# Kernel optimization log

Measured on AMD Instinct MI355X. Metric: run time of the kernel, lower is better.

Reference implementation:

```python
import jax, jax.numpy as jnp
import numpy as np

N_NODES = 50000
N_EDGES = 600000
CHANNELS = 128
HEADS = 8


def setup_inputs() -> dict:
    key = jax.random.key(0)
    k1, k2, k3 = jax.random.split(key, 3)
    x = jax.random.normal(k1, (N_NODES, CHANNELS), dtype=jnp.float32)
    edge_index = jax.random.randint(k2, (2, N_EDGES), 0, N_NODES, dtype=jnp.int32)
    att = jax.random.normal(k3, (HEADS, 2 * (CHANNELS // HEADS)), dtype=jnp.float32)
    return {"x": x, "edge_index": edge_index, "att": att}


def reference(x, edge_index, att):
    # x: [N, C], edge_index: [2, E], att: [H, 2*D] with D = C // H
    src, dst = edge_index[0], edge_index[1]
    n = x.shape[0]
    h = att.shape[0]
    d = att.shape[1] // 2

    x_src = x[src].reshape(-1, h, d)   # [E, H, D]
    x_dst = x[dst].reshape(-1, h, d)   # [E, H, D]

    # (cat([x_src, x_dst]) * att).sum(-1) == x_src @ att[:, :D] + x_dst @ att[:, D:]
    a_src, a_dst = att[:, :d], att[:, d:]
    alpha = jnp.einsum('ehd,hd->eh', x_src, a_src) + jnp.einsum('ehd,hd->eh', x_dst, a_dst)
    alpha = jnp.where(alpha >= 0, alpha, 0.2 * alpha)  # LeakyReLU(0.2)

    # segment softmax over dst; torch scatter_reduce amax includes the zero init,
    # so the per-node max is max(segment_max, 0)
    seg_max = jax.ops.segment_max(alpha, dst, num_segments=n)  # [N, H]
    seg_max = jnp.maximum(seg_max, 0.0)
    alpha = jnp.exp(alpha - seg_max[dst])
    seg_sum = jax.ops.segment_sum(alpha, dst, num_segments=n)  # [N, H]
    alpha = alpha / jnp.maximum(seg_sum[dst], 1e-10)

    # weighted scatter-add of source features
    weighted = x_src * alpha[..., None]                        # [E, H, D]
    out = jax.ops.segment_sum(weighted, dst, num_segments=n)   # [N, H, D]
    return out.reshape(n, -1)
```

## Files before the change

kernel.cpp:

```cpp
#include <hip/hip_runtime.h>

#define N_NODES  50000
#define N_EDGES  600000
#define CHANNELS 128
#define HEADS    8
#define HEAD_DIM 16
#define CAP      64
#define CSTRIDE  4

#define PREP_BLOCK 256
#define SCAT_GRID  ((N_EDGES + PREP_BLOCK - 1) / PREP_BLOCK)
#define LOGIT_GRID ((N_NODES * CHANNELS) / PREP_BLOCK)
#define WPB        4

__global__ void prep_kernel(const float* __restrict__ x,
                            const float* __restrict__ att,
                            const int*   __restrict__ src,
                            const int*   __restrict__ dst,
                            int*            __restrict__ cursor,
                            unsigned short* __restrict__ bucket,
                            float*          __restrict__ ls8,
                            float*          __restrict__ ld8,
                            unsigned short* __restrict__ xb) {
    int b = blockIdx.x;
    if (b < SCAT_GRID) {
        int e = b * PREP_BLOCK + threadIdx.x;
        if (e < N_EDGES) {
            int d = dst[e];
            int pos = atomicAdd(&cursor[d * CSTRIDE], 1);
            if (pos < CAP) bucket[(size_t)d * CAP + pos] = (unsigned short)src[e];
        }
    } else {
        int gid = (b - SCAT_GRID) * PREP_BLOCK + threadIdx.x;
        int n = gid >> 7;
        int c = gid & 127;
        int h = c >> 4;
        int j = c & 15;
        float v = x[gid];

        unsigned int u = __float_as_uint(v);
        xb[gid] = (unsigned short)((u + 0x7FFFu + ((u >> 16) & 1u)) >> 16);

        float ts = v * att[h * (2 * HEAD_DIM) + j];
        float td = v * att[h * (2 * HEAD_DIM) + HEAD_DIM + j];
#pragma unroll
        for (int o = 8; o >= 1; o >>= 1) {
            ts += __shfl_xor(ts, o, 16);
            td += __shfl_xor(td, o, 16);
        }
        if (j == 0) {
            ls8[n * HEADS + h] = ts;
            ld8[n * HEADS + h] = td;
        }
    }
}

__global__ void fused_gat_kernel(const unsigned short* __restrict__ xb,
                                 const float* __restrict__ ls8,
                                 const float* __restrict__ ld8,
                                 const int*   __restrict__ cursor,
                                 const unsigned short* __restrict__ bucket,
                                 float*       __restrict__ out) {
    __shared__ float s_a[WPB * CAP * HEADS];

    int wave = threadIdx.x >> 6;
    int lane = threadIdx.x & 63;
    int n = blockIdx.x * WPB + wave;
    if (n >= N_NODES) return;
    int h = lane >> 3;
    int j = lane & 7;

    int   cnt_raw = cursor[n * CSTRIDE];
    int   myidx   = (int)bucket[(size_t)n * CAP + lane];
    float ldst    = ld8[n * HEADS + h];
    int cnt = (cnt_raw > CAP) ? CAP : cnt_raw;

    float* sa = s_a + wave * (CAP * HEADS);

    float mymax = -1e30f;
    for (int i = j; i < cnt; i += 8) {
        int   s  = __shfl(myidx, i);
        float lg = ls8[s * HEADS + h] + ldst;
        float a  = (lg >= 0.0f) ? lg : 0.2f * lg;
        sa[i * HEADS + h] = a;
        mymax = fmaxf(mymax, a);
    }
#pragma unroll
    for (int o = 4; o >= 1; o >>= 1) mymax = fmaxf(mymax, __shfl_xor(mymax, o, 8));
    float m = fmaxf(mymax, 0.0f);

    float l = 0.0f, accx = 0.0f, accy = 0.0f;
    unsigned int q0 = 0, q1 = 0, q2 = 0;
    if (cnt > 0) {
        int s0 = __shfl(myidx, 0);
        q0 = ((const unsigned int*)(xb + (size_t)s0 * CHANNELS))[lane];
    }
    if (cnt > 1) {
        int s1 = __shfl(myidx, 1);
        q1 = ((const unsigned int*)(xb + (size_t)s1 * CHANNELS))[lane];
    }
    if (cnt > 2) {
        int s2 = __shfl(myidx, 2);
        q2 = ((const unsigned int*)(xb + (size_t)s2 * CHANNELS))[lane];
    }
    for (int i = 0; i < cnt; ++i) {
        unsigned int qc = q0;
        q0 = q1; q1 = q2;
        if (i + 3 < cnt) {
            int s3 = __shfl(myidx, i + 3);
            q2 = ((const unsigned int*)(xb + (size_t)s3 * CHANNELS))[lane];
        }
        float p  = __expf(sa[i * HEADS + h] - m);
        float cx = __uint_as_float(qc << 16);
        float cy = __uint_as_float(qc & 0xFFFF0000u);
        l    += p;
        accx += p * cx;
        accy += p * cy;
    }

    float inv = 1.0f / fmaxf(l, 1e-10f);
    *(float2*)(out + (size_t)n * CHANNELS + 2 * lane) =
        make_float2(accx * inv, accy * inv);
}

extern "C" void kernel_launch(void* const* d_in, const int* in_sizes, int n_in,
                              void* d_out, int out_size, void* d_ws, size_t ws_size,
                              hipStream_t stream) {
    const float* x   = (const float*)d_in[0];
    const int*   ei  = (const int*)  d_in[1];
    const float* att = (const float*)d_in[2];
    const int* src = ei;
    const int* dst = ei + N_EDGES;
    float* out = (float*)d_out;

    int*            cursor = (int*)d_ws;
    unsigned short* bucket = (unsigned short*)(cursor + (size_t)N_NODES * CSTRIDE);
    float*          ls8    = (float*)(bucket + (size_t)N_NODES * CAP);
    float*          ld8    = ls8 + (size_t)N_NODES * HEADS;
    unsigned short* xb     = (unsigned short*)(ld8 + (size_t)N_NODES * HEADS);

    hipMemsetAsync(cursor, 0, sizeof(int) * (size_t)N_NODES * CSTRIDE, stream);

    prep_kernel<<<SCAT_GRID + LOGIT_GRID, PREP_BLOCK, 0, stream>>>(
        x, att, src, dst, cursor, bucket, ls8, ld8, xb);

    {
        int grid = (N_NODES + WPB - 1) / WPB;
        fused_gat_kernel<<<grid, 64 * WPB, 0, stream>>>(
            xb, ls8, ld8, cursor, bucket, out);
    }
}
```

Before: 161.9 us.

## Vectorize prep, batch edge scatter, and deepen gather prefetch in GAT kernel

The prep kernel now processes 4 edges per thread for the bucket scatter and uses float4 loads with ushort4 bf16 stores for the logit/convert path, cutting thread count and shuffle depth. The fused kernel keeps logits in registers, computes exp once in a separate pass and stores probabilities in shared memory, then runs an 8-deep prefetched gather with two accumulator pairs unrolled by 4. This aims to raise memory-level parallelism and remove redundant exp work inside the gather loop, at the cost of more registers and in-flight loads per wave.

```diff
diff --git a/kernel.cpp b/kernel.cpp
--- a/kernel.cpp
+++ b/kernel.cpp
@@ -9,8 +9,10 @@
 #define CSTRIDE  4
 
 #define PREP_BLOCK 256
-#define SCAT_GRID  ((N_EDGES + PREP_BLOCK - 1) / PREP_BLOCK)
-#define LOGIT_GRID ((N_NODES * CHANNELS) / PREP_BLOCK)
+#define EPT        4
+#define SCAT_TH    (N_EDGES / EPT)
+#define SCAT_VB    ((SCAT_TH + PREP_BLOCK - 1) / PREP_BLOCK)
+#define LOGIT_VB   ((N_NODES * (CHANNELS / 4)) / PREP_BLOCK)
 #define WPB        4
 
 __global__ void prep_kernel(const float* __restrict__ x,
@@ -23,32 +25,42 @@
                             float*          __restrict__ ld8,
                             unsigned short* __restrict__ xb) {
     int b = blockIdx.x;
-    if (b < SCAT_GRID) {
-        int e = b * PREP_BLOCK + threadIdx.x;
-        if (e < N_EDGES) {
-            int d = dst[e];
-            int pos = atomicAdd(&cursor[d * CSTRIDE], 1);
-            if (pos < CAP) bucket[(size_t)d * CAP + pos] = (unsigned short)src[e];
+    if (b < SCAT_VB) {
+        int t = b * PREP_BLOCK + threadIdx.x;
+        if (t < SCAT_TH) {
+#pragma unroll
+            for (int k = 0; k < EPT; ++k) {
+                int e = t + k * SCAT_TH;
+                int d = dst[e];
+                int pos = atomicAdd(&cursor[d * CSTRIDE], 1);
+                if (pos < CAP) bucket[(size_t)d * CAP + pos] = (unsigned short)src[e];
+            }
         }
     } else {
-        int gid = (b - SCAT_GRID) * PREP_BLOCK + threadIdx.x;
-        int n = gid >> 7;
-        int c = gid & 127;
-        int h = c >> 4;
-        int j = c & 15;
-        float v = x[gid];
+        int gid = (b - SCAT_VB) * PREP_BLOCK + threadIdx.x;
+        int n  = gid >> 5;
+        int c4 = gid & 31;
+        int h  = c4 >> 2;
+        int j4 = c4 & 3;
 
-        unsigned int u = __float_as_uint(v);
-        xb[gid] = (unsigned short)((u + 0x7FFFu + ((u >> 16) & 1u)) >> 16);
+        float4 v = ((const float4*)x)[gid];
 
-        float ts = v * att[h * (2 * HEAD_DIM) + j];
-        float td = v * att[h * (2 * HEAD_DIM) + HEAD_DIM + j];
-#pragma unroll
-        for (int o = 8; o >= 1; o >>= 1) {
-            ts += __shfl_xor(ts, o, 16);
-            td += __shfl_xor(td, o, 16);
-        }
-        if (j == 0) {
+        unsigned int ux = __float_as_uint(v.x), uy = __float_as_uint(v.y);
+        unsigned int uz = __float_as_uint(v.z), uw = __float_as_uint(v.w);
+        ushort4 pk;
+        pk.x = (unsigned short)((ux + 0x7FFFu + ((ux >> 16) & 1u)) >> 16);
+        pk.y = (unsigned short)((uy + 0x7FFFu + ((uy >> 16) & 1u)) >> 16);
+        pk.z = (unsigned short)((uz + 0x7FFFu + ((uz >> 16) & 1u)) >> 16);
+        pk.w = (unsigned short)((uw + 0x7FFFu + ((uw >> 16) & 1u)) >> 16);
+        ((ushort4*)xb)[gid] = pk;
+
+        float4 as4 = ((const float4*)att)[h * 8 + j4];
+        float4 ad4 = ((const float4*)att)[h * 8 + 4 + j4];
+        float ts = v.x * as4.x + v.y * as4.y + v.z * as4.z + v.w * as4.w;
+        float td = v.x * ad4.x + v.y * ad4.y + v.z * ad4.z + v.w * ad4.w;
+        ts += __shfl_xor(ts, 1, 4); ts += __shfl_xor(ts, 2, 4);
+        td += __shfl_xor(td, 1, 4); td += __shfl_xor(td, 2, 4);
+        if (j4 == 0) {
             ls8[n * HEADS + h] = ts;
             ld8[n * HEADS + h] = td;
         }
@@ -61,7 +73,7 @@
                                  const int*   __restrict__ cursor,
                                  const unsigned short* __restrict__ bucket,
                                  float*       __restrict__ out) {
-    __shared__ float s_a[WPB * CAP * HEADS];
+    __shared__ float s_p[WPB * CAP * HEADS];
 
     int wave = threadIdx.x >> 6;
     int lane = threadIdx.x & 63;
@@ -75,52 +87,72 @@
     float ldst    = ld8[n * HEADS + h];
     int cnt = (cnt_raw > CAP) ? CAP : cnt_raw;
 
-    float* sa = s_a + wave * (CAP * HEADS);
+    float* sp = s_p + wave * (CAP * HEADS);
 
+    float av[8];
     float mymax = -1e30f;
-    for (int i = j; i < cnt; i += 8) {
-        int   s  = __shfl(myidx, i);
-        float lg = ls8[s * HEADS + h] + ldst;
-        float a  = (lg >= 0.0f) ? lg : 0.2f * lg;
-        sa[i * HEADS + h] = a;
-        mymax = fmaxf(mymax, a);
+#pragma unroll
+    for (int k = 0; k < 8; ++k) {
+        int i = j + 8 * k;
+        av[k] = -1e30f;
+        if (i < cnt) {
+            int   s  = __shfl(myidx, i);
+            float lg = ls8[s * HEADS + h] + ldst;
+            float a  = (lg >= 0.0f) ? lg : 0.2f * lg;
+            av[k] = a;
+            mymax = fmaxf(mymax, a);
+        }
     }
 #pragma unroll
     for (int o = 4; o >= 1; o >>= 1) mymax = fmaxf(mymax, __shfl_xor(mymax, o, 8));
     float m = fmaxf(mymax, 0.0f);
 
-    float l = 0.0f, accx = 0.0f, accy = 0.0f;
-    unsigned int q0 = 0, q1 = 0, q2 = 0;
-    if (cnt > 0) {
-        int s0 = __shfl(myidx, 0);
-        q0 = ((const unsigned int*)(xb + (size_t)s0 * CHANNELS))[lane];
+    float myl = 0.0f;
+#pragma unroll
+    for (int k = 0; k < 8; ++k) {
+        int i = j + 8 * k;
+        if (i < cnt) {
+            float p = __expf(av[k] - m);
+            sp[i * HEADS + h] = p;
+            myl += p;
+        }
     }
-    if (cnt > 1) {
-        int s1 = __shfl(myidx, 1);
-        q1 = ((const unsigned int*)(xb + (size_t)s1 * CHANNELS))[lane];
+#pragma unroll
+    for (int o = 4; o >= 1; o >>= 1) myl += __shfl_xor(myl, o, 8);
+
+#define LQ(k) (((k) < cnt) ? ((const unsigned int*)(xb + (size_t)__shfl(myidx,(k)) * CHANNELS))[lane] : 0u)
+    unsigned int q0 = LQ(0), q1 = LQ(1), q2 = LQ(2), q3 = LQ(3);
+    unsigned int q4 = LQ(4), q5 = LQ(5), q6 = LQ(6), q7 = LQ(7);
+
+    float ax0 = 0.f, ay0 = 0.f, ax1 = 0.f, ay1 = 0.f;
+    int i = 0;
+    for (; i + 4 <= cnt; i += 4) {
+        float p0 = sp[(i + 0) * HEADS + h];
+        float p1 = sp[(i + 1) * HEADS + h];
+        float p2 = sp[(i + 2) * HEADS + h];
+        float p3 = sp[(i + 3) * HEADS + h];
+        ax0 += p0 * __uint_as_float(q0 << 16);
+        ay0 += p0 * __uint_as_float(q0 & 0xFFFF0000u);
+        ax1 += p1 * __uint_as_float(q1 << 16);
+        ay1 += p1 * __uint_as_float(q1 & 0xFFFF0000u);
+        ax0 += p2 * __uint_as_float(q2 << 16);
+        ay0 += p2 * __uint_as_float(q2 & 0xFFFF0000u);
+        ax1 += p3 * __uint_as_float(q3 << 16);
+        ay1 += p3 * __uint_as_float(q3 & 0xFFFF0000u);
+        q0 = q4; q1 = q5; q2 = q6; q3 = q7;
+        q4 = LQ(i + 8); q5 = LQ(i + 9); q6 = LQ(i + 10); q7 = LQ(i + 11);
     }
-    if (cnt > 2) {
-        int s2 = __shfl(myidx, 2);
-        q2 = ((const unsigned int*)(xb + (size_t)s2 * CHANNELS))[lane];
+    for (; i < cnt; ++i) {
+        float p = sp[i * HEADS + h];
+        ax0 += p * __uint_as_float(q0 << 16);
+        ay0 += p * __uint_as_float(q0 & 0xFFFF0000u);
+        q0 = q1; q1 = q2; q2 = q3;
     }
-    for (int i = 0; i < cnt; ++i) {
-        unsigned int qc = q0;
-        q0 = q1; q1 = q2;
-        if (i + 3 < cnt) {
-            int s3 = __shfl(myidx, i + 3);
-            q2 = ((const unsigned int*)(xb + (size_t)s3 * CHANNELS))[lane];
-        }
-        float p  = __expf(sa[i * HEADS + h] - m);
-        float cx = __uint_as_float(qc << 16);
-        float cy = __uint_as_float(qc & 0xFFFF0000u);
-        l    += p;
-        accx += p * cx;
-        accy += p * cy;
-    }
+#undef LQ
 
-    float inv = 1.0f / fmaxf(l, 1e-10f);
+    float inv = 1.0f / fmaxf(myl, 1e-10f);
     *(float2*)(out + (size_t)n * CHANNELS + 2 * lane) =
-        make_float2(accx * inv, accy * inv);
+        make_float2((ax0 + ax1) * inv, (ay0 + ay1) * inv);
 }
 
 extern "C" void kernel_launch(void* const* d_in, const int* in_sizes, int n_in,
@@ -141,7 +173,7 @@
 
     hipMemsetAsync(cursor, 0, sizeof(int) * (size_t)N_NODES * CSTRIDE, stream);
 
-    prep_kernel<<<SCAT_GRID + LOGIT_GRID, PREP_BLOCK, 0, stream>>>(
+    prep_kernel<<<SCAT_VB + LOGIT_VB, PREP_BLOCK, 0, stream>>>(
         x, att, src, dst, cursor, bucket, ls8, ld8, xb);
 
     {
```

Result: faster. 146.0 us (-9.8%).
